# Kernel tuning notes

Measured on AMD Instinct MI355X. Metric: run time of the kernel, lower is better.

The kernel has to match this reference:

```python
import jax, jax.numpy as jnp
import numpy as np

N = 100000
D_IN = 512
D_OUT = 512
E = 3200000


def setup_inputs() -> dict:
    key = jax.random.key(0)
    ks = jax.random.split(key, 10)
    stdv = 1.0 / np.sqrt(D_OUT)
    return {
        "x": jax.random.normal(ks[0], (N, D_IN), dtype=jnp.float32),
        "w1": jax.random.uniform(ks[1], (D_IN, D_OUT), jnp.float32, -stdv, stdv),
        "w2": jax.random.uniform(ks[2], (D_IN, D_OUT), jnp.float32, -stdv, stdv),
        "w3": jax.random.uniform(ks[3], (D_IN, D_OUT), jnp.float32, -stdv, stdv),
        "b1": jax.random.uniform(ks[4], (D_OUT,), jnp.float32, -stdv, stdv),
        "b2": jax.random.uniform(ks[5], (D_OUT,), jnp.float32, -stdv, stdv),
        "b3": jax.random.uniform(ks[6], (D_OUT,), jnp.float32, -stdv, stdv),
        "edge_row": jax.random.randint(ks[7], (E,), 0, N, dtype=jnp.int32),
        "edge_col": jax.random.randint(ks[8], (E,), 0, N, dtype=jnp.int32),
        "edge_val": jax.random.uniform(ks[9], (E,), dtype=jnp.float32),
    }


def reference(x, w1, w2, w3, b1, b2, b3, edge_row, edge_col, edge_val):
    n = x.shape[0]
    # three dense projections
    support = x @ w1                      # [N, D_OUT]
    trans = x @ w2 + b2                   # [N, D_OUT]
    gate = jax.nn.sigmoid(x @ w3 + b3)    # [N, D_OUT]
    # sparse adj @ support as edge-list gather -> weighted -> segment_sum
    msgs = support[edge_col] * edge_val[:, None]            # [E, D_OUT]
    agg = jax.ops.segment_sum(msgs, edge_row, num_segments=n)
    out = jax.nn.relu(agg + b1)
    return trans + gate * (out - trans)
```

## Files before the change

### kernel.cpp

```cpp
#include <hip/hip_runtime.h>
#include <hip/hip_bf16.h>
#include <hip/hip_fp16.h>

#define D 512

typedef _Float16 half8 __attribute__((ext_vector_type(8)));
typedef _Float16 half4v __attribute__((ext_vector_type(4)));
typedef float floatx4 __attribute__((ext_vector_type(4)));


__global__ void k_f32_to_f16(const float* __restrict__ in, _Float16* __restrict__ out, int n4) {
  int i = blockIdx.x * blockDim.x + threadIdx.x;
  if (i >= n4) return;
  floatx4 v = __builtin_nontemporal_load((const floatx4*)in + i);
  half4v h;
  h[0] = (_Float16)v[0]; h[1] = (_Float16)v[1]; h[2] = (_Float16)v[2]; h[3] = (_Float16)v[3];
  ((half4v*)out)[i] = h;
}

__global__ void k_build_wt(const float* __restrict__ w1, const float* __restrict__ w2,
                           const float* __restrict__ w3, _Float16* __restrict__ wT) {
  int id = blockIdx.x * blockDim.x + threadIdx.x;
  if (id >= 3 * D * D) return;
  int jg = id >> 9;
  int k  = id & (D - 1);
  const float* w = (jg < D) ? w1 : (jg < 2 * D ? w2 : w3);
  int j = jg & (D - 1);
  wT[id] = (_Float16)w[k * D + j];
}


__global__ void k_count(const int* __restrict__ row, int* __restrict__ counts, int E) {
  int i = blockIdx.x * blockDim.x + threadIdx.x;
  if (i < E) atomicAdd(&counts[row[i]], 1);
}

__global__ __launch_bounds__(256) void k_scan1(const int* __restrict__ in, int* __restrict__ out,
                                               int* __restrict__ bsums, int n) {
  __shared__ int wsum[4];
  int t = threadIdx.x, lane = t & 63, wd = t >> 6;
  int i0 = blockIdx.x * 1024 + t * 4;
  int4 c = make_int4(0, 0, 0, 0);
  if (i0 + 3 < n) c = *(const int4*)(in + i0);
  else {
    if (i0 < n) c.x = in[i0];
    if (i0 + 1 < n) c.y = in[i0 + 1];
    if (i0 + 2 < n) c.z = in[i0 + 2];
  }
  int s1 = c.x, s2 = s1 + c.y, s3 = s2 + c.z, s4 = s3 + c.w;
  int x = s4;
#pragma unroll
  for (int o = 1; o < 64; o <<= 1) { int p = __shfl_up(x, o); if (lane >= o) x += p; }
  if (lane == 63) wsum[wd] = x;
  __syncthreads();
  int wex = 0;
  for (int k = 0; k < wd; ++k) wex += wsum[k];
  int base = wex + x - s4;
  if (i0 + 3 < n) *(int4*)(out + i0) = make_int4(base, base + s1, base + s2, base + s3);
  else {
    if (i0 < n) out[i0] = base;
    if (i0 + 1 < n) out[i0 + 1] = base + s1;
    if (i0 + 2 < n) out[i0 + 2] = base + s2;
  }
  if (t == 0) bsums[blockIdx.x] = wsum[0] + wsum[1] + wsum[2] + wsum[3];
}

__global__ void k_scan2(int* __restrict__ bsums, int* __restrict__ total_out, int nb) {
  __shared__ int w0;
  int t = threadIdx.x, lane = t & 63, wd = t >> 6;
  int v = (t < nb) ? bsums[t] : 0;
  int x = v;
#pragma unroll
  for (int o = 1; o < 64; o <<= 1) { int p = __shfl_up(x, o); if (lane >= o) x += p; }
  if (wd == 0 && lane == 63) w0 = x;
  __syncthreads();
  int excl = x - v + (wd ? w0 : 0);
  if (t < nb) bsums[t] = excl;
  if (t == 127) *total_out = w0 + x;
}

__global__ __launch_bounds__(256) void k_scan3(int* __restrict__ out, const int* __restrict__ bsums, int n) {
  int t = threadIdx.x;
  int i0 = blockIdx.x * 1024 + t * 4;
  int add = bsums[blockIdx.x];
  if (i0 + 3 < n) {
    int4 v = *(int4*)(out + i0);
    v.x += add; v.y += add; v.z += add; v.w += add;
    *(int4*)(out + i0) = v;
  } else {
    for (int k = 0; k < 4; ++k) if (i0 + k < n) out[i0 + k] += add;
  }
}

__global__ void k_scatter(const int* __restrict__ row, const int* __restrict__ col,
                          const float* __restrict__ val, const int* __restrict__ offsets,
                          int* __restrict__ cursor, long long* __restrict__ edges, int E) {
  int i = blockIdx.x * blockDim.x + threadIdx.x;
  if (i >= E) return;
  int r = row[i];
  int c = __builtin_nontemporal_load(col + i);
  float v = __builtin_nontemporal_load(val + i);
  int p = offsets[r] + atomicAdd(&cursor[r], 1);
  long long pack = ((long long)(unsigned)__float_as_int(v) << 32) | (unsigned)c;
  __builtin_nontemporal_store(pack, edges + p);
}

__global__ __launch_bounds__(256) void k_gemm(
    const _Float16* __restrict__ A,
    const _Float16* __restrict__ BT,
    const float* __restrict__ b2, const float* __restrict__ b3,
    _Float16* __restrict__ support, float* __restrict__ trans,
    _Float16* __restrict__ gate, int M)
{
  __shared__ __align__(16) _Float16 ldsA[128 * 32];
  __shared__ __align__(16) _Float16 ldsB[128 * 32];
  int t = threadIdx.x;
  int colBase = blockIdx.x * 128;
  int rowBase = blockIdx.y * 128;
  int w = t >> 6, lane = t & 63, lr = lane & 15, quad = lane >> 4;
  int wrow = (w >> 1) * 64, wcol = (w & 1) * 64;
  floatx4 acc[4][4] = {};

  int srow0 = w * 32 + (lane >> 2);
  int schunk = lane & 3;

  for (int k0 = 0; k0 < D; k0 += 32) {
#pragma unroll
    for (int c = 0; c < 2; ++c) {
      int srow = srow0 + c * 16;
      int chunk = schunk ^ ((srow >> 1) & 3);
      int ga = rowBase + srow; if (ga >= M) ga = M - 1;
      const _Float16* gA = A + (size_t)ga * D + k0 + chunk * 8;
      const _Float16* gB = BT + (size_t)(colBase + srow) * D + k0 + chunk * 8;
      _Float16* lA = &ldsA[(w * 32 + c * 16) * 32];
      _Float16* lB = &ldsB[(w * 32 + c * 16) * 32];
      __builtin_amdgcn_global_load_lds((const __attribute__((address_space(1))) void*)gA,
                                       (__attribute__((address_space(3))) void*)lA, 16, 0, 0);
      __builtin_amdgcn_global_load_lds((const __attribute__((address_space(1))) void*)gB,
                                       (__attribute__((address_space(3))) void*)lB, 16, 0, 0);
    }
    __syncthreads();
    half8 af[4], bf[4];
#pragma unroll
    for (int i2 = 0; i2 < 4; ++i2) {
      int r = wrow + i2 * 16 + lr;
      af[i2] = *(const half8*)&ldsA[r * 32 + ((quad ^ ((r >> 1) & 3)) << 3)];
    }
#pragma unroll
    for (int j = 0; j < 4; ++j) {
      int r = wcol + j * 16 + lr;
      bf[j] = *(const half8*)&ldsB[r * 32 + ((quad ^ ((r >> 1) & 3)) << 3)];
    }
#pragma unroll
    for (int i2 = 0; i2 < 4; ++i2)
#pragma unroll
      for (int j = 0; j < 4; ++j)
        acc[i2][j] = __builtin_amdgcn_mfma_f32_16x16x32_f16(af[i2], bf[j], acc[i2][j], 0, 0, 0);
    __syncthreads();
  }

#pragma unroll
  for (int i2 = 0; i2 < 4; ++i2) {
    int r0 = rowBase + wrow + i2 * 16 + quad * 4;
#pragma unroll
    for (int j = 0; j < 4; ++j) {
      int c = colBase + wcol + j * 16 + lr;
#pragma unroll
      for (int rg = 0; rg < 4; ++rg) {
        int r = r0 + rg;
        if (r >= M) continue;
        float v = acc[i2][j][rg];
        if (c < D) {
          support[(size_t)r * D + c] = (_Float16)v;
        } else if (c < 2 * D) {
          __builtin_nontemporal_store(v + b2[c - D], &trans[(size_t)r * D + (c - D)]);
        } else {
          int cc = c - 2 * D;
          float gv = v + b3[cc];
          gv = 1.0f / (1.0f + __expf(-gv));
          __builtin_nontemporal_store((_Float16)gv, &gate[(size_t)r * D + cc]);
        }
      }
    }
  }
}

__global__ __launch_bounds__(256) void k_agg(
    const _Float16* __restrict__ support, const _Float16* __restrict__ gate,
    float* __restrict__ out, const float* __restrict__ b1,
    const int* __restrict__ offsets, const long long* __restrict__ edges, int n)
{
  int wid = (blockIdx.x * 256 + threadIdx.x) >> 6;
  if (wid >= n) return;
  int lane = threadIdx.x & 63;
  int s = offsets[wid], e = offsets[wid + 1];
  float acc[8] = {0, 0, 0, 0, 0, 0, 0, 0};
  const half8* sup8 = (const half8*)support;

  for (int base = s; base < e; base += 64) {
    int cnt = e - base; if (cnt > 64) cnt = 64;
    int key = 0x7fffffff; float val = 0.f;
    if (lane < cnt) {
      long long ed = __builtin_nontemporal_load(edges + base + lane);
      key = (int)(unsigned)(ed & 0xffffffffll);
      val = __int_as_float((int)(ed >> 32));
    }
#pragma unroll
    for (int size = 2; size <= 64; size <<= 1) {
#pragma unroll
      for (int stride = size >> 1; stride; stride >>= 1) {
        int pk = __shfl_xor(key, stride);
        float pv = __shfl_xor(val, stride);
        bool upper = (lane & stride) != 0;
        bool desc = (lane & size) != 0;
        bool takemax = upper != desc;
        bool swap = takemax ? (pk > key) : (pk < key);
        if (swap) { key = pk; val = pv; }
      }
    }
    int i = 0;
    for (; i + 8 <= cnt; i += 8) {
      int cc[8]; float vv[8];
#pragma unroll
      for (int u = 0; u < 8; ++u) { cc[u] = __shfl(key, i + u); vv[u] = __shfl(val, i + u); }
      half8 h[8];
#pragma unroll
      for (int u = 0; u < 8; ++u) h[u] = sup8[(size_t)cc[u] * 64 + lane];
#pragma unroll
      for (int j = 0; j < 8; ++j) {
        float a = acc[j];
#pragma unroll
        for (int u = 0; u < 8; ++u) a += vv[u] * (float)h[u][j];
        acc[j] = a;
      }
    }
    for (; i + 4 <= cnt; i += 4) {
      int c0 = __shfl(key, i),     c1 = __shfl(key, i + 1);
      int c2 = __shfl(key, i + 2), c3 = __shfl(key, i + 3);
      float v0 = __shfl(val, i),     v1 = __shfl(val, i + 1);
      float v2 = __shfl(val, i + 2), v3 = __shfl(val, i + 3);
      half8 h0 = sup8[(size_t)c0 * 64 + lane];
      half8 h1 = sup8[(size_t)c1 * 64 + lane];
      half8 h2 = sup8[(size_t)c2 * 64 + lane];
      half8 h3 = sup8[(size_t)c3 * 64 + lane];
#pragma unroll
      for (int j = 0; j < 8; ++j)
        acc[j] += v0 * (float)h0[j] + v1 * (float)h1[j] + v2 * (float)h2[j] + v3 * (float)h3[j];
    }
    for (; i < cnt; ++i) {
      int c0 = __shfl(key, i);
      float v0 = __shfl(val, i);
      half8 h0 = sup8[(size_t)c0 * 64 + lane];
#pragma unroll
      for (int j = 0; j < 8; ++j) acc[j] += v0 * (float)h0[j];
    }
  }

  int base4 = wid * 128 + lane * 2;
  floatx4 t0 = __builtin_nontemporal_load((const floatx4*)out + base4);
  floatx4 t1 = __builtin_nontemporal_load((const floatx4*)out + base4 + 1);
  half8 g = __builtin_nontemporal_load((const half8*)gate + (size_t)wid * 64 + lane);
  floatx4 bb0 = ((const floatx4*)b1)[lane * 2];
  floatx4 bb1 = ((const floatx4*)b1)[lane * 2 + 1];
  float tt[8]  = {t0[0], t0[1], t0[2], t0[3], t1[0], t1[1], t1[2], t1[3]};
  float bbv[8] = {bb0[0], bb0[1], bb0[2], bb0[3], bb1[0], bb1[1], bb1[2], bb1[3]};
  float res[8];
#pragma unroll
  for (int j = 0; j < 8; ++j) {
    float o = acc[j] + bbv[j];
    o = o > 0.f ? o : 0.f;
    res[j] = tt[j] + (float)g[j] * (o - tt[j]);
  }
  floatx4 r0, r1;
  r0[0] = res[0]; r0[1] = res[1]; r0[2] = res[2]; r0[3] = res[3];
  r1[0] = res[4]; r1[1] = res[5]; r1[2] = res[6]; r1[3] = res[7];
  __builtin_nontemporal_store(r0, (floatx4*)out + base4);
  __builtin_nontemporal_store(r1, (floatx4*)out + base4 + 1);
}


extern "C" void kernel_launch(void* const* d_in, const int* in_sizes, int n_in,
                              void* d_out, int out_size, void* d_ws, size_t ws_size,
                              hipStream_t stream) {
  const float* x    = (const float*)d_in[0];
  const float* w1   = (const float*)d_in[1];
  const float* w2   = (const float*)d_in[2];
  const float* w3   = (const float*)d_in[3];
  const float* b1   = (const float*)d_in[4];
  const float* b2   = (const float*)d_in[5];
  const float* b3   = (const float*)d_in[6];
  const int*   erow = (const int*)d_in[7];
  const int*   ecol = (const int*)d_in[8];
  const float* eval = (const float*)d_in[9];
  float* out = (float*)d_out;

  int N = in_sizes[0] / D;
  int E = in_sizes[7];

  char* ws = (char*)d_ws;
  size_t off = 0;
  auto take = [&](size_t bytes) -> char* {
    char* p = ws + off;
    off += (bytes + 255) & ~(size_t)255;
    return p;
  };
  _Float16* xh    = (_Float16*)take((size_t)N * D * 2);
  _Float16* wT    = (_Float16*)take((size_t)3 * D * D * 2);
  _Float16* sup   = (_Float16*)take((size_t)N * D * 2);
  _Float16* gate  = (_Float16*)take((size_t)N * D * 2);
  int* counts     = (int*)take((size_t)N * 4);
  int* cursor     = (int*)take((size_t)N * 4);
  int* offsets    = (int*)take((size_t)(N + 1) * 4);
  int* bsums      = (int*)take(128 * 4);
  long long* edges = (long long*)take((size_t)E * 8);

  hipMemsetAsync(counts, 0, (size_t)N * 4, stream);
  hipMemsetAsync(cursor, 0, (size_t)N * 4, stream);

  int n4 = N * D / 4;
  k_f32_to_f16<<<(n4 + 255) / 256, 256, 0, stream>>>(x, xh, n4);
  k_build_wt<<<(3 * D * D + 255) / 256, 256, 0, stream>>>(w1, w2, w3, wT);
  k_count<<<(E + 255) / 256, 256, 0, stream>>>(erow, counts, E);
  int nb = (N + 1023) / 1024;
  k_scan1<<<nb, 256, 0, stream>>>(counts, offsets, bsums, N);
  k_scan2<<<1, 128, 0, stream>>>(bsums, offsets + N, nb);
  k_scan3<<<nb, 256, 0, stream>>>(offsets, bsums, N);
  k_scatter<<<(E + 255) / 256, 256, 0, stream>>>(erow, ecol, eval, offsets, cursor, edges, E);
  dim3 gg(3 * D / 128, (N + 127) / 128);
  k_gemm<<<gg, 256, 0, stream>>>(xh, wT, b2, b3, sup, out, gate, N);
  k_agg<<<((size_t)N * 64 + 255) / 256, 256, 0, stream>>>(sup, gate, out, b1, offsets, edges, N);
}
```

Measured before the change: 1.440 ms.

## Aggregate x before projection and fuse all three GEMMs with epilogue

Uses associativity (A·(xW1) = (A·x)·W1) to run the sparse aggregation on the fp16 input x first, then a single fused GEMM computes agg·W1, x·W2 and x·W3 together and applies bias, relu, sigmoid gate and blend in the epilogue. This removes the fp32 trans write and re-read, the gate write and read, and the support buffer write. In exchange the aggregation output yh is rounded to fp16 before the matmul, which changes numerics, and the GEMM tile is now 128x64 with three accumulator sets, so register pressure and load balance change.

```diff
diff --git a/kernel.cpp b/kernel.cpp
--- a/kernel.cpp
+++ b/kernel.cpp
@@ -105,89 +105,8 @@
   __builtin_nontemporal_store(pack, edges + p);
 }
 
-__global__ __launch_bounds__(256) void k_gemm(
-    const _Float16* __restrict__ A,
-    const _Float16* __restrict__ BT,
-    const float* __restrict__ b2, const float* __restrict__ b3,
-    _Float16* __restrict__ support, float* __restrict__ trans,
-    _Float16* __restrict__ gate, int M)
-{
-  __shared__ __align__(16) _Float16 ldsA[128 * 32];
-  __shared__ __align__(16) _Float16 ldsB[128 * 32];
-  int t = threadIdx.x;
-  int colBase = blockIdx.x * 128;
-  int rowBase = blockIdx.y * 128;
-  int w = t >> 6, lane = t & 63, lr = lane & 15, quad = lane >> 4;
-  int wrow = (w >> 1) * 64, wcol = (w & 1) * 64;
-  floatx4 acc[4][4] = {};
-
-  int srow0 = w * 32 + (lane >> 2);
-  int schunk = lane & 3;
-
-  for (int k0 = 0; k0 < D; k0 += 32) {
-#pragma unroll
-    for (int c = 0; c < 2; ++c) {
-      int srow = srow0 + c * 16;
-      int chunk = schunk ^ ((srow >> 1) & 3);
-      int ga = rowBase + srow; if (ga >= M) ga = M - 1;
-      const _Float16* gA = A + (size_t)ga * D + k0 + chunk * 8;
-      const _Float16* gB = BT + (size_t)(colBase + srow) * D + k0 + chunk * 8;
-      _Float16* lA = &ldsA[(w * 32 + c * 16) * 32];
-      _Float16* lB = &ldsB[(w * 32 + c * 16) * 32];
-      __builtin_amdgcn_global_load_lds((const __attribute__((address_space(1))) void*)gA,
-                                       (__attribute__((address_space(3))) void*)lA, 16, 0, 0);
-      __builtin_amdgcn_global_load_lds((const __attribute__((address_space(1))) void*)gB,
-                                       (__attribute__((address_space(3))) void*)lB, 16, 0, 0);
-    }
-    __syncthreads();
-    half8 af[4], bf[4];
-#pragma unroll
-    for (int i2 = 0; i2 < 4; ++i2) {
-      int r = wrow + i2 * 16 + lr;
-      af[i2] = *(const half8*)&ldsA[r * 32 + ((quad ^ ((r >> 1) & 3)) << 3)];
-    }
-#pragma unroll
-    for (int j = 0; j < 4; ++j) {
-      int r = wcol + j * 16 + lr;
-      bf[j] = *(const half8*)&ldsB[r * 32 + ((quad ^ ((r >> 1) & 3)) << 3)];
-    }
-#pragma unroll
-    for (int i2 = 0; i2 < 4; ++i2)
-#pragma unroll
-      for (int j = 0; j < 4; ++j)
-        acc[i2][j] = __builtin_amdgcn_mfma_f32_16x16x32_f16(af[i2], bf[j], acc[i2][j], 0, 0, 0);
-    __syncthreads();
-  }
-
-#pragma unroll
-  for (int i2 = 0; i2 < 4; ++i2) {
-    int r0 = rowBase + wrow + i2 * 16 + quad * 4;
-#pragma unroll
-    for (int j = 0; j < 4; ++j) {
-      int c = colBase + wcol + j * 16 + lr;
-#pragma unroll
-      for (int rg = 0; rg < 4; ++rg) {
-        int r = r0 + rg;
-        if (r >= M) continue;
-        float v = acc[i2][j][rg];
-        if (c < D) {
-          support[(size_t)r * D + c] = (_Float16)v;
-        } else if (c < 2 * D) {
-          __builtin_nontemporal_store(v + b2[c - D], &trans[(size_t)r * D + (c - D)]);
-        } else {
-          int cc = c - 2 * D;
-          float gv = v + b3[cc];
-          gv = 1.0f / (1.0f + __expf(-gv));
-          __builtin_nontemporal_store((_Float16)gv, &gate[(size_t)r * D + cc]);
-        }
-      }
-    }
-  }
-}
-
 __global__ __launch_bounds__(256) void k_agg(
-    const _Float16* __restrict__ support, const _Float16* __restrict__ gate,
-    float* __restrict__ out, const float* __restrict__ b1,
+    const _Float16* __restrict__ xh, _Float16* __restrict__ yh,
     const int* __restrict__ offsets, const long long* __restrict__ edges, int n)
 {
   int wid = (blockIdx.x * 256 + threadIdx.x) >> 6;
@@ -195,7 +114,7 @@
   int lane = threadIdx.x & 63;
   int s = offsets[wid], e = offsets[wid + 1];
   float acc[8] = {0, 0, 0, 0, 0, 0, 0, 0};
-  const half8* sup8 = (const half8*)support;
+  const half8* x8 = (const half8*)xh;
 
   for (int base = s; base < e; base += 64) {
     int cnt = e - base; if (cnt > 64) cnt = 64;
@@ -225,7 +144,7 @@
       for (int u = 0; u < 8; ++u) { cc[u] = __shfl(key, i + u); vv[u] = __shfl(val, i + u); }
       half8 h[8];
 #pragma unroll
-      for (int u = 0; u < 8; ++u) h[u] = sup8[(size_t)cc[u] * 64 + lane];
+      for (int u = 0; u < 8; ++u) h[u] = x8[(size_t)cc[u] * 64 + lane];
 #pragma unroll
       for (int j = 0; j < 8; ++j) {
         float a = acc[j];
@@ -239,10 +158,10 @@
       int c2 = __shfl(key, i + 2), c3 = __shfl(key, i + 3);
       float v0 = __shfl(val, i),     v1 = __shfl(val, i + 1);
       float v2 = __shfl(val, i + 2), v3 = __shfl(val, i + 3);
-      half8 h0 = sup8[(size_t)c0 * 64 + lane];
-      half8 h1 = sup8[(size_t)c1 * 64 + lane];
-      half8 h2 = sup8[(size_t)c2 * 64 + lane];
-      half8 h3 = sup8[(size_t)c3 * 64 + lane];
+      half8 h0 = x8[(size_t)c0 * 64 + lane];
+      half8 h1 = x8[(size_t)c1 * 64 + lane];
+      half8 h2 = x8[(size_t)c2 * 64 + lane];
+      half8 h3 = x8[(size_t)c3 * 64 + lane];
 #pragma unroll
       for (int j = 0; j < 8; ++j)
         acc[j] += v0 * (float)h0[j] + v1 * (float)h1[j] + v2 * (float)h2[j] + v3 * (float)h3[j];
@@ -250,32 +169,110 @@
     for (; i < cnt; ++i) {
       int c0 = __shfl(key, i);
       float v0 = __shfl(val, i);
-      half8 h0 = sup8[(size_t)c0 * 64 + lane];
+      half8 h0 = x8[(size_t)c0 * 64 + lane];
 #pragma unroll
       for (int j = 0; j < 8; ++j) acc[j] += v0 * (float)h0[j];
     }
   }
 
-  int base4 = wid * 128 + lane * 2;
-  floatx4 t0 = __builtin_nontemporal_load((const floatx4*)out + base4);
-  floatx4 t1 = __builtin_nontemporal_load((const floatx4*)out + base4 + 1);
-  half8 g = __builtin_nontemporal_load((const half8*)gate + (size_t)wid * 64 + lane);
-  floatx4 bb0 = ((const floatx4*)b1)[lane * 2];
-  floatx4 bb1 = ((const floatx4*)b1)[lane * 2 + 1];
-  float tt[8]  = {t0[0], t0[1], t0[2], t0[3], t1[0], t1[1], t1[2], t1[3]};
-  float bbv[8] = {bb0[0], bb0[1], bb0[2], bb0[3], bb1[0], bb1[1], bb1[2], bb1[3]};
-  float res[8];
-#pragma unroll
-  for (int j = 0; j < 8; ++j) {
-    float o = acc[j] + bbv[j];
-    o = o > 0.f ? o : 0.f;
-    res[j] = tt[j] + (float)g[j] * (o - tt[j]);
-  }
-  floatx4 r0, r1;
-  r0[0] = res[0]; r0[1] = res[1]; r0[2] = res[2]; r0[3] = res[3];
-  r1[0] = res[4]; r1[1] = res[5]; r1[2] = res[6]; r1[3] = res[7];
-  __builtin_nontemporal_store(r0, (floatx4*)out + base4);
-  __builtin_nontemporal_store(r1, (floatx4*)out + base4 + 1);
+  half8 o;
+#pragma unroll
+  for (int j = 0; j < 8; ++j) o[j] = (_Float16)acc[j];
+  ((half8*)yh)[(size_t)wid * 64 + lane] = o;
+}
+
+__global__ __launch_bounds__(256) void k_gemm_fused(
+    const _Float16* __restrict__ Ax,
+    const _Float16* __restrict__ Ay,
+    const _Float16* __restrict__ BT,
+    const float* __restrict__ b1, const float* __restrict__ b2,
+    const float* __restrict__ b3, float* __restrict__ out, int M)
+{
+  __shared__ __align__(16) _Float16 ldsAx[128 * 32];
+  __shared__ __align__(16) _Float16 ldsAy[128 * 32];
+  __shared__ __align__(16) _Float16 ldsB[192 * 32];
+  int t = threadIdx.x;
+  int cb = blockIdx.x;
+  int rowBase = blockIdx.y * 128;
+  int w = t >> 6, lane = t & 63, lr = lane & 15, quad = lane >> 4;
+  floatx4 acc[3][2][4] = {};
+
+  int srow0 = lane >> 2;
+  int schunk = lane & 3;
+
+  for (int k0 = 0; k0 < D; k0 += 32) {
+#pragma unroll
+    for (int c = 0; c < 2; ++c) {
+      int srow = w * 32 + c * 16 + srow0;
+      int chunk = schunk ^ ((srow >> 1) & 3);
+      int ga = rowBase + srow; if (ga >= M) ga = M - 1;
+      const _Float16* gx = Ax + (size_t)ga * D + k0 + chunk * 8;
+      const _Float16* gy = Ay + (size_t)ga * D + k0 + chunk * 8;
+      _Float16* lx = &ldsAx[(w * 32 + c * 16) * 32];
+      _Float16* ly = &ldsAy[(w * 32 + c * 16) * 32];
+      __builtin_amdgcn_global_load_lds((const __attribute__((address_space(1))) void*)gx,
+                                       (__attribute__((address_space(3))) void*)lx, 16, 0, 0);
+      __builtin_amdgcn_global_load_lds((const __attribute__((address_space(1))) void*)gy,
+                                       (__attribute__((address_space(3))) void*)ly, 16, 0, 0);
+    }
+#pragma unroll
+    for (int c = 0; c < 3; ++c) {
+      int srow = w * 48 + c * 16 + srow0;
+      int chunk = schunk ^ ((srow >> 1) & 3);
+      int m = srow >> 6, j = srow & 63;
+      const _Float16* gB = BT + (size_t)(m * 512 + cb * 64 + j) * D + k0 + chunk * 8;
+      _Float16* lB = &ldsB[(w * 48 + c * 16) * 32];
+      __builtin_amdgcn_global_load_lds((const __attribute__((address_space(1))) void*)gB,
+                                       (__attribute__((address_space(3))) void*)lB, 16, 0, 0);
+    }
+    __syncthreads();
+
+    half8 afx[2], afy[2];
+#pragma unroll
+    for (int i2 = 0; i2 < 2; ++i2) {
+      int r = w * 32 + i2 * 16 + lr;
+      int sl = (quad ^ ((r >> 1) & 3)) << 3;
+      afx[i2] = *(const half8*)&ldsAx[r * 32 + sl];
+      afy[i2] = *(const half8*)&ldsAy[r * 32 + sl];
+    }
+#pragma unroll
+    for (int m = 0; m < 3; ++m) {
+      half8 bf[4];
+#pragma unroll
+      for (int f = 0; f < 4; ++f) {
+        int r = m * 64 + f * 16 + lr;
+        bf[f] = *(const half8*)&ldsB[r * 32 + ((quad ^ ((r >> 1) & 3)) << 3)];
+      }
+#pragma unroll
+      for (int i2 = 0; i2 < 2; ++i2)
+#pragma unroll
+        for (int f = 0; f < 4; ++f)
+          acc[m][i2][f] = __builtin_amdgcn_mfma_f32_16x16x32_f16(
+              m == 0 ? afy[i2] : afx[i2], bf[f], acc[m][i2][f], 0, 0, 0);
+    }
+    __syncthreads();
+  }
+
+#pragma unroll
+  for (int i2 = 0; i2 < 2; ++i2) {
+    int r0 = rowBase + w * 32 + i2 * 16 + quad * 4;
+#pragma unroll
+    for (int f = 0; f < 4; ++f) {
+      int c = cb * 64 + f * 16 + lr;
+      float bb1 = b1[c], bb2 = b2[c], bb3 = b3[c];
+#pragma unroll
+      for (int rg = 0; rg < 4; ++rg) {
+        int r = r0 + rg;
+        if (r >= M) continue;
+        float aggv = acc[0][i2][f][rg] + bb1;
+        aggv = aggv > 0.f ? aggv : 0.f;
+        float tr = acc[1][i2][f][rg] + bb2;
+        float gv = acc[2][i2][f][rg] + bb3;
+        gv = 1.0f / (1.0f + __expf(-gv));
+        __builtin_nontemporal_store(tr + gv * (aggv - tr), &out[(size_t)r * D + c]);
+      }
+    }
+  }
 }
 
 
@@ -305,9 +302,8 @@
     return p;
   };
   _Float16* xh    = (_Float16*)take((size_t)N * D * 2);
+  _Float16* yh    = (_Float16*)take((size_t)N * D * 2);
   _Float16* wT    = (_Float16*)take((size_t)3 * D * D * 2);
-  _Float16* sup   = (_Float16*)take((size_t)N * D * 2);
-  _Float16* gate  = (_Float16*)take((size_t)N * D * 2);
   int* counts     = (int*)take((size_t)N * 4);
   int* cursor     = (int*)take((size_t)N * 4);
   int* offsets    = (int*)take((size_t)(N + 1) * 4);
@@ -326,7 +322,7 @@
   k_scan2<<<1, 128, 0, stream>>>(bsums, offsets + N, nb);
   k_scan3<<<nb, 256, 0, stream>>>(offsets, bsums, N);
   k_scatter<<<(E + 255) / 256, 256, 0, stream>>>(erow, ecol, eval, offsets, cursor, edges, E);
-  dim3 gg(3 * D / 128, (N + 127) / 128);
-  k_gemm<<<gg, 256, 0, stream>>>(xh, wT, b2, b3, sup, out, gate, N);
-  k_agg<<<((size_t)N * 64 + 255) / 256, 256, 0, stream>>>(sup, gate, out, b1, offsets, edges, N);
-}
+  k_agg<<<((size_t)N * 64 + 255) / 256, 256, 0, stream>>>(xh, yh, offsets, edges, N);
+  dim3 gg(D / 64, (N + 127) / 128);
+  k_gemm_fused<<<gg, 256, 0, stream>>>(xh, yh, wT, b1, b2, b3, out, N);
+}
```

New measurement: 1.369 ms. 4.9% less time.
